# Performance work log

Hardware: AMD Instinct MI355X
Metric: run time of the kernel (lower is better)

Reference implementation:

```python
import jax, jax.numpy as jnp
from jax import lax
import numpy as np

B, L, D = 32, 128, 6          # programs, statements per program, tree depth
T = 2 ** D - 1                # nodes per statement tree (complete binary tree)
V, E, C, H = 50000, 128, 128, 256  # vocab, embed dim, encode dim, gru hidden


def setup_inputs():
    key = jax.random.key(0)
    ks = jax.random.split(key, 12)
    s = 0.05
    return {
        "tokens": jax.random.randint(ks[0], (B, L, T), 0, V),
        "emb": jax.random.normal(ks[1], (V, E), jnp.float32) * s,
        "Wc": jax.random.normal(ks[2], (C, E), jnp.float32) * s,
        "bc": jax.random.normal(ks[3], (C,), jnp.float32) * s,
        "Wih_f": jax.random.normal(ks[4], (3 * H, C), jnp.float32) * s,
        "Whh_f": jax.random.normal(ks[5], (3 * H, H), jnp.float32) * s,
        "bih_f": jax.random.normal(ks[6], (3 * H,), jnp.float32) * s,
        "bhh_f": jax.random.normal(ks[7], (3 * H,), jnp.float32) * s,
        "Wih_b": jax.random.normal(ks[8], (3 * H, C), jnp.float32) * s,
        "Whh_b": jax.random.normal(ks[9], (3 * H, H), jnp.float32) * s,
        "bih_b": jax.random.normal(ks[10], (3 * H,), jnp.float32) * s,
        "bhh_b": jax.random.normal(ks[11], (3 * H,), jnp.float32) * s,
    }


def _tree_encode(tokens, emb, Wc, bc):
    # h(node) = W_c(embed(tok)) + sum of children subtree encodings (W_l/W_r unused in source)
    h = jnp.einsum("blte,ce->bltc", emb[tokens], Wc) + bc  # [B,L,T,C]
    for d in range(D - 1, 0, -1):  # deepest level first
        start, n = 2 ** d - 1, 2 ** d
        ch = h[:, :, start:start + n, :]
        ch = ch.reshape(ch.shape[0], ch.shape[1], n // 2, 2, ch.shape[-1]).sum(3)
        p0 = 2 ** (d - 1) - 1
        h = h.at[:, :, p0:p0 + n // 2, :].add(ch)
    # max over all subtree encodings, with zeros included (batch_node starts at 0)
    return jnp.maximum(h.max(axis=2), 0.0)  # [B,L,C]


def _gru_dir(x, Wih, Whh, bih, bhh, reverse):
    # torch GRU gate order: r, z, n
    def step(hp, xt):
        gi = xt @ Wih.T + bih
        gh = hp @ Whh.T + bhh
        ir, iz, inn = jnp.split(gi, 3, -1)
        hr, hz, hn = jnp.split(gh, 3, -1)
        r = jax.nn.sigmoid(ir + hr)
        z = jax.nn.sigmoid(iz + hz)
        nn_ = jnp.tanh(inn + r * hn)
        hnew = (1.0 - z) * nn_ + z * hp
        return hnew, hnew
    xs = jnp.swapaxes(x, 0, 1)  # [L,B,C]
    h0 = jnp.zeros((x.shape[0], Whh.shape[1]), x.dtype)
    _, ys = lax.scan(step, h0, xs, reverse=reverse)
    return jnp.swapaxes(ys, 0, 1)  # [B,L,H]


def reference(tokens, emb, Wc, bc, Wih_f, Whh_f, bih_f, bhh_f, Wih_b, Whh_b, bih_b, bhh_b):
    enc = _tree_encode(tokens, emb, Wc, bc)                       # [B,L,C]
    fwd = _gru_dir(enc, Wih_f, Whh_f, bih_f, bhh_f, reverse=False)
    bwd = _gru_dir(enc, Wih_b, Whh_b, bih_b, bhh_b, reverse=True)
    gru_out = jnp.concatenate([fwd, bwd], axis=-1)                # [B,L,2H]
    return gru_out.max(axis=1)                                    # max-pool over time -> [B,2H]
```

## Files before the change

kernel.cpp:

```cpp
#include <hip/hip_runtime.h>
#include <hip/hip_bf16.h>
#include <hip/hip_fp16.h>
#include <math.h>

#define NV 50000
#define NC 128
#define NH 256
#define NB 32
#define NL 128
#define NT 63
#define G3 768

typedef _Float16 half2_t __attribute__((ext_vector_type(2)));

__device__ __forceinline__ float sigmoidf_(float x) { return 1.0f / (1.0f + expf(-x)); }

__device__ __forceinline__ float fdot2_(unsigned int a, unsigned int b, float c) {
#if __has_builtin(__builtin_amdgcn_fdot2)
  return __builtin_amdgcn_fdot2(__builtin_bit_cast(half2_t, a),
                                __builtin_bit_cast(half2_t, b), c, false);
#else
  half2_t ah = __builtin_bit_cast(half2_t, a);
  half2_t bh = __builtin_bit_cast(half2_t, b);
  return fmaf((float)ah[0], (float)bh[0], fmaf((float)ah[1], (float)bh[1], c));
#endif
}

__device__ __forceinline__ float dpp_xor1_add(float v) {
  int x = __builtin_amdgcn_update_dpp(0, __builtin_bit_cast(int, v),
                                      0xB1, 0xF, 0xF, true);
  return v + __builtin_bit_cast(float, x);
}

__global__ __launch_bounds__(256) void gemm_bt_k128(
    const float* __restrict__ A, const float* __restrict__ Bm,
    const float* __restrict__ bias, float* __restrict__ Cm,
    int M, int N) {
  __shared__ __align__(16) float As[64 * 129];
  __shared__ __align__(16) float BsT[64 * 132];
  const int m0 = blockIdx.x * 64;
  const int n0 = blockIdx.y * 128;
  const int tid = threadIdx.x;

#pragma unroll
  for (int i = 0; i < 32; ++i) {
    int e = tid + i * 256;
    int r = e >> 7, k = e & 127;
    int m = m0 + r;
    As[r * 129 + k] = (m < M) ? A[(size_t)m * 128 + k] : 0.0f;
  }

  const int tn = tid & 15;
  const int tm = tid >> 4;
  const int ml = tm * 4, nl = tn * 8;

  float acc[4][8];
#pragma unroll
  for (int i = 0; i < 4; ++i)
#pragma unroll
    for (int j = 0; j < 8; ++j) acc[i][j] = 0.0f;

#pragma unroll
  for (int h = 0; h < 2; ++h) {
    if (h) __syncthreads();
#pragma unroll
    for (int i = 0; i < 32; ++i) {
      int e = tid + i * 256;
      int n = e >> 6, kk = e & 63;
      BsT[kk * 132 + n] = Bm[(size_t)(n0 + n) * 128 + h * 64 + kk];
    }
    __syncthreads();
#pragma unroll 4
    for (int kk = 0; kk < 64; ++kk) {
      const int k = h * 64 + kk;
      float a0 = As[(ml + 0) * 129 + k];
      float a1 = As[(ml + 1) * 129 + k];
      float a2 = As[(ml + 2) * 129 + k];
      float a3 = As[(ml + 3) * 129 + k];
      float4 b0 = *(const float4*)&BsT[kk * 132 + nl];
      float4 b1 = *(const float4*)&BsT[kk * 132 + nl + 4];
      const float bv[8] = {b0.x, b0.y, b0.z, b0.w, b1.x, b1.y, b1.z, b1.w};
#pragma unroll
      for (int j = 0; j < 8; ++j) {
        acc[0][j] = fmaf(a0, bv[j], acc[0][j]);
        acc[1][j] = fmaf(a1, bv[j], acc[1][j]);
        acc[2][j] = fmaf(a2, bv[j], acc[2][j]);
        acc[3][j] = fmaf(a3, bv[j], acc[3][j]);
      }
    }
  }

  float bv[8];
#pragma unroll
  for (int j = 0; j < 8; ++j) bv[j] = bias ? bias[n0 + nl + j] : 0.0f;

#pragma unroll
  for (int i = 0; i < 4; ++i) {
    int m = m0 + ml + i;
    if (m < M) {
      float* crow = &Cm[(size_t)m * N + n0 + nl];
#pragma unroll
      for (int j = 0; j < 8; ++j) crow[j] = acc[i][j] + bv[j];
    }
  }
}

__global__ __launch_bounds__(256) void gemm_bt_k128_dual(
    const float* __restrict__ A,
    const float* __restrict__ B0, const float* __restrict__ B1,
    const float* __restrict__ bias0, const float* __restrict__ bias1,
    float* __restrict__ C0, float* __restrict__ C1, int M, int N) {
  const float* __restrict__ Bm = blockIdx.z ? B1 : B0;
  const float* __restrict__ bias = blockIdx.z ? bias1 : bias0;
  float* __restrict__ Cm = blockIdx.z ? C1 : C0;

  __shared__ __align__(16) float As[64 * 129];
  __shared__ __align__(16) float BsT[64 * 132];
  const int m0 = blockIdx.x * 64;
  const int n0 = blockIdx.y * 128;
  const int tid = threadIdx.x;

#pragma unroll
  for (int i = 0; i < 32; ++i) {
    int e = tid + i * 256;
    int r = e >> 7, k = e & 127;
    int m = m0 + r;
    As[r * 129 + k] = (m < M) ? A[(size_t)m * 128 + k] : 0.0f;
  }

  const int tn = tid & 15;
  const int tm = tid >> 4;
  const int ml = tm * 4, nl = tn * 8;

  float acc[4][8];
#pragma unroll
  for (int i = 0; i < 4; ++i)
#pragma unroll
    for (int j = 0; j < 8; ++j) acc[i][j] = 0.0f;

#pragma unroll
  for (int h = 0; h < 2; ++h) {
    if (h) __syncthreads();
#pragma unroll
    for (int i = 0; i < 32; ++i) {
      int e = tid + i * 256;
      int n = e >> 6, kk = e & 63;
      BsT[kk * 132 + n] = Bm[(size_t)(n0 + n) * 128 + h * 64 + kk];
    }
    __syncthreads();
#pragma unroll 4
    for (int kk = 0; kk < 64; ++kk) {
      const int k = h * 64 + kk;
      float a0 = As[(ml + 0) * 129 + k];
      float a1 = As[(ml + 1) * 129 + k];
      float a2 = As[(ml + 2) * 129 + k];
      float a3 = As[(ml + 3) * 129 + k];
      float4 b0 = *(const float4*)&BsT[kk * 132 + nl];
      float4 b1 = *(const float4*)&BsT[kk * 132 + nl + 4];
      const float bv[8] = {b0.x, b0.y, b0.z, b0.w, b1.x, b1.y, b1.z, b1.w};
#pragma unroll
      for (int j = 0; j < 8; ++j) {
        acc[0][j] = fmaf(a0, bv[j], acc[0][j]);
        acc[1][j] = fmaf(a1, bv[j], acc[1][j]);
        acc[2][j] = fmaf(a2, bv[j], acc[2][j]);
        acc[3][j] = fmaf(a3, bv[j], acc[3][j]);
      }
    }
  }

  float bv[8];
#pragma unroll
  for (int j = 0; j < 8; ++j) bv[j] = bias[n0 + nl + j];

#pragma unroll
  for (int i = 0; i < 4; ++i) {
    int m = m0 + ml + i;
    if (m < M) {
      float* crow = &Cm[(size_t)m * N + n0 + nl];
#pragma unroll
      for (int j = 0; j < 8; ++j) crow[j] = acc[i][j] + bv[j];
    }
  }
}

__global__ __launch_bounds__(128) void tree_encode(
    const int* __restrict__ tokens, const float* __restrict__ P,
    const float* __restrict__ bc, float* __restrict__ enc) {
  __shared__ int toks[NT];
  const int blk = blockIdx.x;
  const int c = threadIdx.x;
  if (c < NT) toks[c] = tokens[(size_t)blk * NT + c];
  __syncthreads();

  float s[NT];
#pragma unroll
  for (int i = 0; i < NT; ++i) s[i] = P[(size_t)toks[i] * NC + c];
#pragma unroll
  for (int i = 30; i >= 0; --i) s[i] += s[2 * i + 1] + s[2 * i + 2];

  const float bcv = bc[c];
  float m = -1e30f;
#pragma unroll
  for (int i = 0; i < NT; ++i) {
    const float cnt = (i == 0) ? 63.0f
                    : (i < 3)  ? 31.0f
                    : (i < 7)  ? 15.0f
                    : (i < 15) ? 7.0f
                    : (i < 31) ? 3.0f
                               : 1.0f;
    m = fmaxf(m, s[i] + cnt * bcv);
  }
  enc[(size_t)blk * NC + c] = fmaxf(m, 0.0f);
}

__global__ __launch_bounds__(256) void conv_w_pack(
    const float* __restrict__ Wf, const float* __restrict__ Wb,
    uint4* __restrict__ out) {
  int i = blockIdx.x * 256 + threadIdx.x;
  if (i >= 2 * 48 * 512) return;
  const int dir = i / 24576;
  int rem = i - dir * 24576;
  const int q = rem >> 9;
  const int tid = rem & 511;
  const int g = q >> 4;
  const int j = q & 15;
  const int c = tid >> 1;
  const int kh = tid & 1;
  const int row = g * 256 + c;
  const int k0 = kh * 128 + j * 8;
  const float* __restrict__ W = dir ? Wb : Wf;
  const float4 a = *(const float4*)&W[(size_t)row * NH + k0];
  const float4 b = *(const float4*)&W[(size_t)row * NH + k0 + 4];
  __half2 p0 = __floats2half2_rn(a.x, a.y);
  __half2 p1 = __floats2half2_rn(a.z, a.w);
  __half2 p2 = __floats2half2_rn(b.x, b.y);
  __half2 p3 = __floats2half2_rn(b.z, b.w);
  uint4 o;
  o.x = *(unsigned int*)&p0; o.y = *(unsigned int*)&p1;
  o.z = *(unsigned int*)&p2; o.w = *(unsigned int*)&p3;
  out[i] = o;
}

__global__ __launch_bounds__(512, 2) void gru_scan_v7(
    const uint4* __restrict__ Wpk, const float* __restrict__ GI,
    const float* __restrict__ bhh_f, const float* __restrict__ bhh_b,
    float* __restrict__ out) {
  const int dir = blockIdx.x >> 5;
  const int b = blockIdx.x & 31;
  const int tid = threadIdx.x;
  const int c = tid >> 1;
  const int kh = tid & 1;

  __shared__ __align__(16) uint4 hbuf[2][34];

  const uint4* __restrict__ Wd = Wpk + (size_t)dir * 48 * 512;
  uint4 w[48];
#pragma unroll
  for (int q = 0; q < 48; ++q) w[q] = Wd[(size_t)q * 512 + tid];
#pragma unroll
  for (int q = 0; q < 48; ++q)
    asm volatile("" : "+v"(w[q].x), "+v"(w[q].y), "+v"(w[q].z), "+v"(w[q].w));

  const float* __restrict__ bhh = dir ? bhh_b : bhh_f;
  const float br = bhh[c], bz = bhh[c + NH], bn = bhh[c + 2 * NH];
  if (tid < 136) ((unsigned int*)hbuf)[tid] = 0u;

  const float* __restrict__ gi_base =
      GI + ((size_t)dir * NB * NL + (size_t)b * NL) * G3;
  float gir, giz, gin;
  {
    const float* g = gi_base + (size_t)(dir ? NL - 1 : 0) * G3;
    gir = g[c]; giz = g[c + NH]; gin = g[c + 2 * NH];
  }
  float hreg = 0.0f, hmax = -1e30f;
  const int hidx = c + ((c >> 7) << 3);
  __syncthreads();

  for (int st = 0; st < NL; ++st) {
    float girN, gizN, ginN;
    {
      const int stn = (st + 1 < NL) ? st + 1 : st;
      const int t = dir ? (NL - 1 - stn) : stn;
      const float* g = gi_base + (size_t)t * G3;
      girN = g[c]; gizN = g[c + NH]; ginN = g[c + 2 * NH];
    }
    const uint4* __restrict__ hp = hbuf[st & 1] + kh * 17;
    float ar = 0.f, az = 0.f, an = 0.f;
#pragma unroll
    for (int j = 0; j < 16; ++j) {
      uint4 hv = hp[j];
      ar = fdot2_(w[j].x, hv.x, ar);       ar = fdot2_(w[j].y, hv.y, ar);
      ar = fdot2_(w[j].z, hv.z, ar);       ar = fdot2_(w[j].w, hv.w, ar);
      az = fdot2_(w[16 + j].x, hv.x, az);  az = fdot2_(w[16 + j].y, hv.y, az);
      az = fdot2_(w[16 + j].z, hv.z, az);  az = fdot2_(w[16 + j].w, hv.w, az);
      an = fdot2_(w[32 + j].x, hv.x, an);  an = fdot2_(w[32 + j].y, hv.y, an);
      an = fdot2_(w[32 + j].z, hv.z, an);  an = fdot2_(w[32 + j].w, hv.w, an);
    }
    ar = dpp_xor1_add(ar);
    az = dpp_xor1_add(az);
    an = dpp_xor1_add(an);
    float r = sigmoidf_(gir + ar + br);
    float z = sigmoidf_(giz + az + bz);
    float n = tanhf(gin + r * (an + bn));
    hreg = (1.0f - z) * n + z * hreg;
    hmax = fmaxf(hmax, hreg);
    if (kh == 0) {
      ((unsigned short*)&hbuf[(st + 1) & 1][0])[hidx] =
          __half_as_ushort(__float2half_rn(hreg));
    }
    __syncthreads();
    gir = girN; giz = gizN; gin = ginN;
  }
  if (kh == 0) out[(size_t)b * (2 * NH) + (size_t)dir * NH + c] = hmax;
}

extern "C" void kernel_launch(void* const* d_in, const int* in_sizes, int n_in,
                              void* d_out, int out_size, void* d_ws, size_t ws_size,
                              hipStream_t stream) {
  const int*   tokens = (const int*)d_in[0];
  const float* emb    = (const float*)d_in[1];
  const float* Wc     = (const float*)d_in[2];
  const float* bc     = (const float*)d_in[3];
  const float* Wih_f  = (const float*)d_in[4];
  const float* Whh_f  = (const float*)d_in[5];
  const float* bih_f  = (const float*)d_in[6];
  const float* bhh_f  = (const float*)d_in[7];
  const float* Wih_b  = (const float*)d_in[8];
  const float* Whh_b  = (const float*)d_in[9];
  const float* bih_b  = (const float*)d_in[10];
  const float* bhh_b  = (const float*)d_in[11];
  float* out = (float*)d_out;

  float* P   = (float*)d_ws;
  float* enc = P + (size_t)NV * NC;
  float* GI  = enc + (size_t)NB * NL * NC;
  uint4* Wpk = (uint4*)(GI + (size_t)2 * NB * NL * G3);

  conv_w_pack<<<dim3((2 * 48 * 512 + 255) / 256), dim3(256), 0, stream>>>(
      Whh_f, Whh_b, Wpk);
  gemm_bt_k128<<<dim3((NV + 63) / 64, NC / 128), dim3(256), 0, stream>>>(
      emb, Wc, nullptr, P, NV, NC);
  tree_encode<<<dim3(NB * NL), dim3(128), 0, stream>>>(tokens, P, bc, enc);
  gemm_bt_k128_dual<<<dim3(NB * NL / 64, G3 / 128, 2), dim3(256), 0, stream>>>(
      enc, Wih_f, Wih_b, bih_f, bih_b,
      GI, GI + (size_t)NB * NL * G3, NB * NL, G3);
  gru_scan_v7<<<dim3(64), dim3(512), 0, stream>>>(
      Wpk, GI, bhh_f, bhh_b, out);
}
```

Baseline: 296.0 us.

## Split GRU recurrence across four threads per hidden unit with reloaded gate weights

The GRU scan now uses 1024 threads per block, with four threads sharing each hidden unit's dot product and reducing through two DPP steps instead of one. Only the reset-gate weights stay in registers. The update and new-gate weights are reloaded from global memory (cache) on every time step to cut register pressure. The aim is a shorter serial dot-product chain per step, at the cost of repeated weight loads inside the latency-critical loop and more idle lanes in the gate math.

```diff
diff --git a/kernel.cpp b/kernel.cpp
--- a/kernel.cpp
+++ b/kernel.cpp
@@ -28,7 +28,12 @@
 
 __device__ __forceinline__ float dpp_xor1_add(float v) {
   int x = __builtin_amdgcn_update_dpp(0, __builtin_bit_cast(int, v),
-                                      0xB1, 0xF, 0xF, true);
+                                      0xB1 , 0xF, 0xF, true);
+  return v + __builtin_bit_cast(float, x);
+}
+__device__ __forceinline__ float dpp_xor2_add(float v) {
+  int x = __builtin_amdgcn_update_dpp(0, __builtin_bit_cast(int, v),
+                                      0x4E , 0xF, 0xF, true);
   return v + __builtin_bit_cast(float, x);
 }
 
@@ -217,17 +222,17 @@
     const float* __restrict__ Wf, const float* __restrict__ Wb,
     uint4* __restrict__ out) {
   int i = blockIdx.x * 256 + threadIdx.x;
-  if (i >= 2 * 48 * 512) return;
+  if (i >= 2 * 24 * 1024) return;
   const int dir = i / 24576;
   int rem = i - dir * 24576;
-  const int q = rem >> 9;
-  const int tid = rem & 511;
-  const int g = q >> 4;
-  const int j = q & 15;
-  const int c = tid >> 1;
-  const int kh = tid & 1;
+  const int j = rem >> 10;
+  const int tid = rem & 1023;
+  const int g = j >> 3;
+  const int jj = j & 7;
+  const int c = tid >> 2;
+  const int kq = tid & 3;
   const int row = g * 256 + c;
-  const int k0 = kh * 128 + j * 8;
+  const int k0 = kq * 64 + jj * 8;
   const float* __restrict__ W = dir ? Wb : Wf;
   const float4 a = *(const float4*)&W[(size_t)row * NH + k0];
   const float4 b = *(const float4*)&W[(size_t)row * NH + k0 + 4];
@@ -241,77 +246,85 @@
   out[i] = o;
 }
 
-__global__ __launch_bounds__(512, 2) void gru_scan_v7(
+__global__ __launch_bounds__(1024, 4) void gru_scan_v8(
     const uint4* __restrict__ Wpk, const float* __restrict__ GI,
     const float* __restrict__ bhh_f, const float* __restrict__ bhh_b,
     float* __restrict__ out) {
   const int dir = blockIdx.x >> 5;
   const int b = blockIdx.x & 31;
   const int tid = threadIdx.x;
-  const int c = tid >> 1;
-  const int kh = tid & 1;
-
-  __shared__ __align__(16) uint4 hbuf[2][34];
-
-  const uint4* __restrict__ Wd = Wpk + (size_t)dir * 48 * 512;
-  uint4 w[48];
-#pragma unroll
-  for (int q = 0; q < 48; ++q) w[q] = Wd[(size_t)q * 512 + tid];
-#pragma unroll
-  for (int q = 0; q < 48; ++q)
-    asm volatile("" : "+v"(w[q].x), "+v"(w[q].y), "+v"(w[q].z), "+v"(w[q].w));
-
+  const int c = tid >> 2;
+  const int kq = tid & 3;
+
+  __shared__ __align__(16) uint4 hbuf[2][36];
+
+  const uint4* __restrict__ Wd = Wpk + (size_t)dir * 24 * 1024;
+
+  uint4 wr[8];
+#pragma unroll
+  for (int jj = 0; jj < 8; ++jj) wr[jj] = Wd[(size_t)jj * 1024 + tid];
+#pragma unroll
+  for (int jj = 0; jj < 8; ++jj)
+    asm volatile("" : "+v"(wr[jj].x), "+v"(wr[jj].y), "+v"(wr[jj].z), "+v"(wr[jj].w));
+
+  const bool own = (kq == 0);
   const float* __restrict__ bhh = dir ? bhh_b : bhh_f;
-  const float br = bhh[c], bz = bhh[c + NH], bn = bhh[c + 2 * NH];
-  if (tid < 136) ((unsigned int*)hbuf)[tid] = 0u;
+  float br = 0.f, bz = 0.f, bn = 0.f;
+  if (own) { br = bhh[c]; bz = bhh[c + NH]; bn = bhh[c + 2 * NH]; }
+  if (tid < 144) ((unsigned int*)hbuf)[tid] = 0u;
 
   const float* __restrict__ gi_base =
       GI + ((size_t)dir * NB * NL + (size_t)b * NL) * G3;
-  float gir, giz, gin;
-  {
+  float gir = 0.f, giz = 0.f, gin = 0.f;
+  if (own) {
     const float* g = gi_base + (size_t)(dir ? NL - 1 : 0) * G3;
     gir = g[c]; giz = g[c + NH]; gin = g[c + 2 * NH];
   }
   float hreg = 0.0f, hmax = -1e30f;
-  const int hidx = c + ((c >> 7) << 3);
+  const int hidx = (c >> 6) * 72 + (c & 63);
   __syncthreads();
 
   for (int st = 0; st < NL; ++st) {
-    float girN, gizN, ginN;
-    {
+    uint4 wz[8], wn[8];
+#pragma unroll
+    for (int jj = 0; jj < 8; ++jj) wz[jj] = Wd[(size_t)(8 + jj) * 1024 + tid];
+#pragma unroll
+    for (int jj = 0; jj < 8; ++jj) wn[jj] = Wd[(size_t)(16 + jj) * 1024 + tid];
+    float girN = 0.f, gizN = 0.f, ginN = 0.f;
+    if (own) {
       const int stn = (st + 1 < NL) ? st + 1 : st;
       const int t = dir ? (NL - 1 - stn) : stn;
       const float* g = gi_base + (size_t)t * G3;
       girN = g[c]; gizN = g[c + NH]; ginN = g[c + 2 * NH];
     }
-    const uint4* __restrict__ hp = hbuf[st & 1] + kh * 17;
+    const uint4* __restrict__ hp = hbuf[st & 1] + kq * 9;
     float ar = 0.f, az = 0.f, an = 0.f;
 #pragma unroll
-    for (int j = 0; j < 16; ++j) {
-      uint4 hv = hp[j];
-      ar = fdot2_(w[j].x, hv.x, ar);       ar = fdot2_(w[j].y, hv.y, ar);
-      ar = fdot2_(w[j].z, hv.z, ar);       ar = fdot2_(w[j].w, hv.w, ar);
-      az = fdot2_(w[16 + j].x, hv.x, az);  az = fdot2_(w[16 + j].y, hv.y, az);
-      az = fdot2_(w[16 + j].z, hv.z, az);  az = fdot2_(w[16 + j].w, hv.w, az);
-      an = fdot2_(w[32 + j].x, hv.x, an);  an = fdot2_(w[32 + j].y, hv.y, an);
-      an = fdot2_(w[32 + j].z, hv.z, an);  an = fdot2_(w[32 + j].w, hv.w, an);
-    }
-    ar = dpp_xor1_add(ar);
-    az = dpp_xor1_add(az);
-    an = dpp_xor1_add(an);
-    float r = sigmoidf_(gir + ar + br);
-    float z = sigmoidf_(giz + az + bz);
-    float n = tanhf(gin + r * (an + bn));
-    hreg = (1.0f - z) * n + z * hreg;
-    hmax = fmaxf(hmax, hreg);
-    if (kh == 0) {
+    for (int jj = 0; jj < 8; ++jj) {
+      uint4 hv = hp[jj];
+      ar = fdot2_(wr[jj].x, hv.x, ar);  ar = fdot2_(wr[jj].y, hv.y, ar);
+      ar = fdot2_(wr[jj].z, hv.z, ar);  ar = fdot2_(wr[jj].w, hv.w, ar);
+      az = fdot2_(wz[jj].x, hv.x, az);  az = fdot2_(wz[jj].y, hv.y, az);
+      az = fdot2_(wz[jj].z, hv.z, az);  az = fdot2_(wz[jj].w, hv.w, az);
+      an = fdot2_(wn[jj].x, hv.x, an);  an = fdot2_(wn[jj].y, hv.y, an);
+      an = fdot2_(wn[jj].z, hv.z, an);  an = fdot2_(wn[jj].w, hv.w, an);
+    }
+    ar = dpp_xor2_add(dpp_xor1_add(ar));
+    az = dpp_xor2_add(dpp_xor1_add(az));
+    an = dpp_xor2_add(dpp_xor1_add(an));
+    if (own) {
+      float r = sigmoidf_(gir + ar + br);
+      float z = sigmoidf_(giz + az + bz);
+      float n = tanhf(gin + r * (an + bn));
+      hreg = (1.0f - z) * n + z * hreg;
+      hmax = fmaxf(hmax, hreg);
       ((unsigned short*)&hbuf[(st + 1) & 1][0])[hidx] =
           __half_as_ushort(__float2half_rn(hreg));
     }
     __syncthreads();
     gir = girN; giz = gizN; gin = ginN;
   }
-  if (kh == 0) out[(size_t)b * (2 * NH) + (size_t)dir * NH + c] = hmax;
+  if (own) out[(size_t)b * (2 * NH) + (size_t)dir * NH + c] = hmax;
 }
 
 extern "C" void kernel_launch(void* const* d_in, const int* in_sizes, int n_in,
@@ -336,7 +349,7 @@
   float* GI  = enc + (size_t)NB * NL * NC;
   uint4* Wpk = (uint4*)(GI + (size_t)2 * NB * NL * G3);
 
-  conv_w_pack<<<dim3((2 * 48 * 512 + 255) / 256), dim3(256), 0, stream>>>(
+  conv_w_pack<<<dim3((2 * 24 * 1024 + 255) / 256), dim3(256), 0, stream>>>(
       Whh_f, Whh_b, Wpk);
   gemm_bt_k128<<<dim3((NV + 63) / 64, NC / 128), dim3(256), 0, stream>>>(
       emb, Wc, nullptr, P, NV, NC);
@@ -344,6 +357,6 @@
   gemm_bt_k128_dual<<<dim3(NB * NL / 64, G3 / 128, 2), dim3(256), 0, stream>>>(
       enc, Wih_f, Wih_b, bih_f, bih_b,
       GI, GI + (size_t)NB * NL * G3, NB * NL, G3);
-  gru_scan_v7<<<dim3(64), dim3(512), 0, stream>>>(
+  gru_scan_v8<<<dim3(64), dim3(1024), 0, stream>>>(
       Wpk, GI, bhh_f, bhh_b, out);
 }
```

Result: slower. 367.3 us (+24.1%).
